# Kernel tuning notes

Measured on AMD Instinct MI355X. Metric: run time of the kernel, lower is better.

The kernel has to match this reference:

```python
import jax, jax.numpy as jnp
import numpy as np

B, S, D, H, DFF = 2, 2048, 512, 8, 2048
DH = D // H
EPS = 1e-5


def setup_inputs() -> dict:
    key = jax.random.key(0)
    ks = jax.random.split(key, 12)
    g = lambda k, shape, s=0.02: jax.random.normal(k, shape, dtype=jnp.float32) * s
    x = jax.random.normal(ks[0], (B, S, D), dtype=jnp.float32)
    # additive causal mask: 0 on/below diag, -inf above
    neg = jnp.finfo(jnp.float32).min
    attn_mask = jnp.where(jnp.tril(jnp.ones((S, S), dtype=bool)), 0.0, neg).astype(jnp.float32)
    return {
        "x": x,
        "attn_mask": attn_mask,
        "Wq": g(ks[1], (D, D)), "bq": jnp.zeros((D,), jnp.float32),
        "Wk": g(ks[2], (D, D)), "bk": jnp.zeros((D,), jnp.float32),
        "Wv": g(ks[3], (D, D)), "bv": jnp.zeros((D,), jnp.float32),
        "Wo": g(ks[4], (D, D)), "bo": jnp.zeros((D,), jnp.float32),
        "head_alphas": jnp.ones((H,), jnp.float32),
        "ln1_g": jnp.ones((D,), jnp.float32), "ln1_b": jnp.zeros((D,), jnp.float32),
        "W1": g(ks[5], (DFF, D)), "b1": jnp.zeros((DFF,), jnp.float32),
        "W2": g(ks[6], (D, DFF)), "b2": jnp.zeros((D,), jnp.float32),
        "ln2_g": jnp.ones((D,), jnp.float32), "ln2_b": jnp.zeros((D,), jnp.float32),
    }


def _layer_norm(h, g, b):
    mu = jnp.mean(h, axis=-1, keepdims=True)
    var = jnp.mean((h - mu) ** 2, axis=-1, keepdims=True)
    return (h - mu) * jax.lax.rsqrt(var + EPS) * g + b


def reference(x, attn_mask, Wq, bq, Wk, bk, Wv, bv, Wo, bo, head_alphas,
              ln1_g, ln1_b, W1, b1, W2, b2, ln2_g, ln2_b):
    scale = jnp.sqrt(jnp.asarray(DH, dtype=x.dtype))
    # projections (torch Linear: x @ W.T + b)
    q = (x @ Wq.T + bq).reshape(B, S, H, DH).transpose(0, 2, 1, 3)  # bhsd
    k = (x @ Wk.T + bk).reshape(B, S, H, DH).transpose(0, 2, 1, 3)
    v = (x @ Wv.T + bv).reshape(B, S, H, DH).transpose(0, 2, 1, 3)
    attn = jnp.einsum('bhqd,bhkd->bhqk', q, k) / scale
    attn = attn + attn_mask  # broadcast [S,S] over batch/heads
    attn = jax.nn.softmax(attn, axis=-1)
    ctx = jnp.einsum('bhqk,bhkd->bhqd', attn, v)
    ctx = ctx * head_alphas[None, :, None, None]
    ctx = ctx.transpose(0, 2, 1, 3).reshape(B, S, D)
    attn_out = ctx @ Wo.T + bo
    # residual + LN
    h = _layer_norm(x + attn_out, ln1_g, ln1_b)
    # FFN (linear -> ReLU -> linear), residual + LN
    ff = jax.nn.relu(h @ W1.T + b1) @ W2.T + b2
    out = _layer_norm(h + ff, ln2_g, ln2_b)
    return out
```

## Files before the change

kernel.cpp:

```cpp
#include <hip/hip_runtime.h>
#include <hip/hip_bf16.h>
#include <math.h>

#define BB 2
#define SS 2048
#define DD 512
#define HH 8
#define DH 64
#define DFF 2048
#define MM (BB*SS)
#define EPS 1e-5f

typedef __attribute__((ext_vector_type(8))) short bf16x8;
typedef __attribute__((ext_vector_type(4))) float f32x4;

#define GL2LDS(g, l)                                                        \
    __builtin_amdgcn_global_load_lds(                                       \
        (const __attribute__((address_space(1))) void*)(unsigned long long)(g), \
        (__attribute__((address_space(3))) void*)(unsigned int)(unsigned long long)(l), \
        16, 0, 0)

struct Cvt7 {
    const float* s[7];
    unsigned short* d[7];
    unsigned off[8];
};

__global__ __launch_bounds__(256) void cvt_k(Cvt7 a)
{
    unsigned i = blockIdx.x * 256 + threadIdx.x;
    int seg = 0;
    #pragma unroll
    for (int t = 1; t < 7; ++t) seg += (i >= a.off[t]);
    unsigned li = i - a.off[seg];
    float4 v = ((const float4*)a.s[seg])[li];
    union { __hip_bfloat16 h[4]; uint2 u; } t;
    t.h[0] = __float2bfloat16(v.x);
    t.h[1] = __float2bfloat16(v.y);
    t.h[2] = __float2bfloat16(v.z);
    t.h[3] = __float2bfloat16(v.w);
    ((uint2*)a.d[seg])[li] = t.u;
}

__global__ __launch_bounds__(256) void gemm64_k(
    const __hip_bfloat16* __restrict__ A, const __hip_bfloat16* __restrict__ Bw,
    const float* __restrict__ bias, const float* __restrict__ resid,
    void* __restrict__ Cout, int N_, int K_, int mode, float oscale)
{
    __shared__ __hip_bfloat16 As[64*64];
    __shared__ __hip_bfloat16 Bs[64*64];
    const int tid   = threadIdx.x;
    const int w     = tid >> 6;
    const int lane  = tid & 63;
    const int quad  = lane >> 4;
    const int col16 = lane & 15;
    const int m0 = blockIdx.y * 64;
    const int n0 = blockIdx.x * 64;
    const int wm = (w >> 1) * 32;
    const int wn = (w & 1) * 32;
    const int srow = lane >> 3;
    const int scol = (lane & 7) * 8;

    f32x4 acc[2][2] = {};

    for (int k0 = 0; k0 < K_; k0 += 64) {
        __syncthreads();
        #pragma unroll
        for (int t = 0; t < 4; ++t) {
            const int c = w * 4 + t;
            if (c < 8)
                GL2LDS(A  + (size_t)(m0 + c*8 + srow) * K_ + k0 + scol,
                       (char*)As + c * 1024);
            else
                GL2LDS(Bw + (size_t)(n0 + (c-8)*8 + srow) * K_ + k0 + scol,
                       (char*)Bs + (c-8) * 1024);
        }
        __syncthreads();

        #pragma unroll
        for (int kk = 0; kk < 64; kk += 32) {
            bf16x8 af[2], bf[2];
            #pragma unroll
            for (int i = 0; i < 2; ++i)
                af[i] = *(const bf16x8*)(As + (wm + i*16 + col16) * 64 + kk + quad*8);
            #pragma unroll
            for (int j = 0; j < 2; ++j)
                bf[j] = *(const bf16x8*)(Bs + (wn + j*16 + col16) * 64 + kk + quad*8);
            #pragma unroll
            for (int i = 0; i < 2; ++i)
                #pragma unroll
                for (int j = 0; j < 2; ++j)
                    acc[i][j] = __builtin_amdgcn_mfma_f32_16x16x32_bf16(
                        af[i], bf[j], acc[i][j], 0, 0, 0);
        }
    }

    #pragma unroll
    for (int i = 0; i < 2; ++i) {
        #pragma unroll
        for (int r = 0; r < 4; ++r) {
            const int m = m0 + wm + i*16 + quad*4 + r;
            #pragma unroll
            for (int j = 0; j < 2; ++j) {
                const int n = n0 + wn + j*16 + col16;
                float vv = acc[i][j][r] + bias[n];
                if (mode == 0) {
                    size_t idx = (size_t)m * N_ + n;
                    float* Cf = (float*)Cout;
                    if (resid) vv += resid[idx];
                    Cf[idx] = vv;
                } else {
                    ((__hip_bfloat16*)Cout)[(size_t)m * N_ + n] =
                        __float2bfloat16(fmaxf(vv, 0.f) * oscale);
                }
            }
        }
    }
}

__global__ __launch_bounds__(256) void gemm64sk_k(
    const __hip_bfloat16* __restrict__ A, const __hip_bfloat16* __restrict__ Bw,
    float* __restrict__ part, int N_, int Ktot, int Kseg)
{
    __shared__ __hip_bfloat16 As[64*64];
    __shared__ __hip_bfloat16 Bs[64*64];
    const int tid   = threadIdx.x;
    const int w     = tid >> 6;
    const int lane  = tid & 63;
    const int quad  = lane >> 4;
    const int col16 = lane & 15;
    const int m0 = blockIdx.y * 64;
    const int n0 = blockIdx.x * 64;
    const int wm = (w >> 1) * 32;
    const int wn = (w & 1) * 32;
    const int srow = lane >> 3;
    const int scol = (lane & 7) * 8;
    const int kbeg = blockIdx.z * Kseg;

    f32x4 acc[2][2] = {};

    for (int k0 = kbeg; k0 < kbeg + Kseg; k0 += 64) {
        __syncthreads();
        #pragma unroll
        for (int t = 0; t < 4; ++t) {
            const int c = w * 4 + t;
            if (c < 8)
                GL2LDS(A  + (size_t)(m0 + c*8 + srow) * Ktot + k0 + scol,
                       (char*)As + c * 1024);
            else
                GL2LDS(Bw + (size_t)(n0 + (c-8)*8 + srow) * Ktot + k0 + scol,
                       (char*)Bs + (c-8) * 1024);
        }
        __syncthreads();

        #pragma unroll
        for (int kk = 0; kk < 64; kk += 32) {
            bf16x8 af[2], bf[2];
            #pragma unroll
            for (int i = 0; i < 2; ++i)
                af[i] = *(const bf16x8*)(As + (wm + i*16 + col16) * 64 + kk + quad*8);
            #pragma unroll
            for (int j = 0; j < 2; ++j)
                bf[j] = *(const bf16x8*)(Bs + (wn + j*16 + col16) * 64 + kk + quad*8);
            #pragma unroll
            for (int i = 0; i < 2; ++i)
                #pragma unroll
                for (int j = 0; j < 2; ++j)
                    acc[i][j] = __builtin_amdgcn_mfma_f32_16x16x32_bf16(
                        af[i], bf[j], acc[i][j], 0, 0, 0);
        }
    }

    float* dst = part + (size_t)blockIdx.z * MM * N_;
    #pragma unroll
    for (int i = 0; i < 2; ++i)
        #pragma unroll
        for (int r = 0; r < 4; ++r) {
            const int m = m0 + wm + i*16 + quad*4 + r;
            #pragma unroll
            for (int j = 0; j < 2; ++j) {
                const int n = n0 + wn + j*16 + col16;
                dst[(size_t)m * N_ + n] = acc[i][j][r];
            }
        }
}

__global__ __launch_bounds__(256) void qkv64_k(
    const __hip_bfloat16* __restrict__ A, const __hip_bfloat16* __restrict__ Wqkv,
    const float* __restrict__ bq, const float* __restrict__ bk,
    const float* __restrict__ bv,
    __hip_bfloat16* __restrict__ qb, __hip_bfloat16* __restrict__ kb,
    __hip_bfloat16* __restrict__ vtb)
{
    __shared__ __hip_bfloat16 As[64*64];
    __shared__ __hip_bfloat16 Bs[64*64];
    const int tid   = threadIdx.x;
    const int w     = tid >> 6;
    const int lane  = tid & 63;
    const int quad  = lane >> 4;
    const int col16 = lane & 15;
    const int m0 = blockIdx.y * 64;
    const int n0 = blockIdx.x * 64;
    const int wm = (w >> 1) * 32;
    const int wn = (w & 1) * 32;
    const int srow = lane >> 3;
    const int scol = (lane & 7) * 8;

    f32x4 acc[2][2] = {};

    for (int k0 = 0; k0 < DD; k0 += 64) {
        __syncthreads();
        #pragma unroll
        for (int t = 0; t < 4; ++t) {
            const int c = w * 4 + t;
            if (c < 8)
                GL2LDS(A    + (size_t)(m0 + c*8 + srow) * DD + k0 + scol,
                       (char*)As + c * 1024);
            else
                GL2LDS(Wqkv + (size_t)(n0 + (c-8)*8 + srow) * DD + k0 + scol,
                       (char*)Bs + (c-8) * 1024);
        }
        __syncthreads();

        #pragma unroll
        for (int kk = 0; kk < 64; kk += 32) {
            bf16x8 af[2], bf[2];
            #pragma unroll
            for (int i = 0; i < 2; ++i)
                af[i] = *(const bf16x8*)(As + (wm + i*16 + col16) * 64 + kk + quad*8);
            #pragma unroll
            for (int j = 0; j < 2; ++j)
                bf[j] = *(const bf16x8*)(Bs + (wn + j*16 + col16) * 64 + kk + quad*8);
            #pragma unroll
            for (int i = 0; i < 2; ++i)
                #pragma unroll
                for (int j = 0; j < 2; ++j)
                    acc[i][j] = __builtin_amdgcn_mfma_f32_16x16x32_bf16(
                        af[i], bf[j], acc[i][j], 0, 0, 0);
        }
    }

    const int z = n0 >> 9;
    const float* bias = (z == 0) ? bq : (z == 1) ? bk : bv;
    __hip_bfloat16* dst = (z == 0) ? qb : (z == 1) ? kb : vtb;
    const float sc = (z == 0) ? 0.125f : 1.0f;
    #pragma unroll
    for (int i = 0; i < 2; ++i)
        #pragma unroll
        for (int r = 0; r < 4; ++r) {
            const int m = m0 + wm + i*16 + quad*4 + r;
            const int b = m >> 11, s = m & (SS - 1);
            #pragma unroll
            for (int j = 0; j < 2; ++j) {
                const int n  = n0 + wn + j*16 + col16;
                const int nn = n & 511;
                const int hh = nn >> 6, d = nn & (DH - 1);
                float vv = (acc[i][j][r] + bias[nn]) * sc;
                if (z < 2)
                    dst[(((size_t)(b*HH + hh))*SS + s)*DH + d] = __float2bfloat16(vv);
                else
                    dst[(((size_t)(b*HH + hh))*DH + d)*SS + s] = __float2bfloat16(vv);
            }
        }
}

__global__ __launch_bounds__(512) void attn_mfma_k(
    const __hip_bfloat16* __restrict__ Q,
    const __hip_bfloat16* __restrict__ K,
    const __hip_bfloat16* __restrict__ VT,
    const float* __restrict__ halpha,
    __hip_bfloat16* __restrict__ ctx)
{
    const int w    = threadIdx.x >> 6;
    const int lane = threadIdx.x & 63;
    const int quad = lane >> 4;
    const int col  = lane & 15;
    const int bh   = blockIdx.x;
    const int b    = bh >> 3, h = bh & 7;
    const int qt   = gridDim.y - 1 - blockIdx.y;
    const int q0   = qt * 64;
    const int nchunk = qt + 1;

    const __hip_bfloat16* Qbh = Q  + (size_t)bh * SS * DH;
    const __hip_bfloat16* Kbh = K  + (size_t)bh * SS * DH;
    const __hip_bfloat16* Vbh = VT + (size_t)bh * DH * SS;

    __shared__ float smem[16896];
    __hip_bfloat16* bb     = (__hip_bfloat16*)smem;
    __hip_bfloat16* p_base = bb + (size_t)w * 4096;
    float* lbuf = smem + 16384;

    bf16x8 qf[4][2];
    #pragma unroll
    for (int mi = 0; mi < 4; ++mi) {
        const __hip_bfloat16* qp = Qbh + (size_t)(q0 + mi*16 + col) * DH + quad * 8;
        qf[mi][0] = *(const bf16x8*)(qp);
        qf[mi][1] = *(const bf16x8*)(qp + 32);
    }

    f32x4 acc_o[4][4] = {};
    float lp[4][4] = {};

    for (int c = w; c < nchunk; c += 8) {
        const int k0 = c * 64;
        const bool diag = (c == qt);

        #pragma unroll
        for (int ks = 0; ks < 4; ++ks) {
            const __hip_bfloat16* kp = Kbh + (size_t)(k0 + ks*16 + col) * DH + quad * 8;
            bf16x8 kb0 = *(const bf16x8*)(kp);
            bf16x8 kb1 = *(const bf16x8*)(kp + 32);
            const int keyl = ks*16 + col;
            const int kh = keyl >> 5;
            const int lr = ((keyl >> 3) & 3) * 16;
            const int j  = keyl & 7;
            const int kg = k0 + keyl;
            #pragma unroll
            for (int mi = 0; mi < 4; ++mi) {
                f32x4 s = {};
                s = __builtin_amdgcn_mfma_f32_16x16x32_bf16(qf[mi][0], kb0, s, 0, 0, 0);
                s = __builtin_amdgcn_mfma_f32_16x16x32_bf16(qf[mi][1], kb1, s, 0, 0, 0);
                #pragma unroll
                for (int r = 0; r < 4; ++r) {
                    float p;
                    if (diag) {
                        int qg = q0 + mi*16 + quad*4 + r;
                        p = (kg > qg) ? 0.f : __expf(s[r]);
                    } else {
                        p = __expf(s[r]);
                    }
                    lp[mi][r] += p;
                    p_base[mi*1024 + kh*512 + (lr + quad*4 + r)*8 + j] =
                        __float2bfloat16(p);
                }
            }
        }

        bf16x8 pa[4][2];
        #pragma unroll
        for (int mi = 0; mi < 4; ++mi) {
            pa[mi][0] = *(const bf16x8*)(p_base + mi*1024 + lane*8);
            pa[mi][1] = *(const bf16x8*)(p_base + mi*1024 + 512 + lane*8);
        }
        #pragma unroll
        for (int d = 0; d < 4; ++d) {
            const __hip_bfloat16* vp = Vbh + (size_t)(d*16 + col) * SS + k0 + quad * 8;
            bf16x8 vb0 = *(const bf16x8*)(vp);
            bf16x8 vb1 = *(const bf16x8*)(vp + 32);
            #pragma unroll
            for (int mi = 0; mi < 4; ++mi) {
                acc_o[mi][d] = __builtin_amdgcn_mfma_f32_16x16x32_bf16(pa[mi][0], vb0, acc_o[mi][d], 0, 0, 0);
                acc_o[mi][d] = __builtin_amdgcn_mfma_f32_16x16x32_bf16(pa[mi][1], vb1, acc_o[mi][d], 0, 0, 0);
            }
        }
    }

    #pragma unroll
    for (int mi = 0; mi < 4; ++mi)
        #pragma unroll
        for (int r = 0; r < 4; ++r) {
            float s_ = lp[mi][r];
            #pragma unroll
            for (int o = 1; o < 16; o <<= 1) s_ += __shfl_xor(s_, o);
            lp[mi][r] = s_;
        }

    __syncthreads();
    __hip_bfloat16* obuf = bb + (size_t)w * 4096;
    #pragma unroll
    for (int mi = 0; mi < 4; ++mi)
        #pragma unroll
        for (int d = 0; d < 4; ++d)
            #pragma unroll
            for (int r = 0; r < 4; ++r)
                obuf[(mi*16 + quad*4 + r)*64 + d*16 + col] =
                    __float2bfloat16(acc_o[mi][d][r]);
    if (col == 0) {
        #pragma unroll
        for (int mi = 0; mi < 4; ++mi)
            #pragma unroll
            for (int r = 0; r < 4; ++r)
                lbuf[w*64 + mi*16 + quad*4 + r] = lp[mi][r];
    }
    __syncthreads();

    const float ha = halpha[h];
    #pragma unroll
    for (int rr = 0; rr < 8; ++rr) {
        const int row = w*8 + rr;
        float L = 0.f, val = 0.f;
        #pragma unroll
        for (int p = 0; p < 8; ++p) {
            L   += lbuf[p*64 + row];
            val += __bfloat162float(bb[p*4096 + row*64 + lane]);
        }
        ctx[((size_t)(b*SS + q0 + row))*DD + h*64 + lane] =
            __float2bfloat16(val * ha / L);
    }
}

__global__ __launch_bounds__(256) void ln_red_k(
    const float* __restrict__ pa, const float* __restrict__ pb,
    const float* __restrict__ bias, const float* __restrict__ resid,
    const float* __restrict__ g, const float* __restrict__ bta,
    float* __restrict__ out, __hip_bfloat16* __restrict__ outb)
{
    const int row = blockIdx.x;
    const size_t base = (size_t)row * DD;
    const int t = threadIdx.x;
    float v0 = pa[base + t]       + pb[base + t]       + bias[t]       + resid[base + t];
    float v1 = pa[base + t + 256] + pb[base + t + 256] + bias[t + 256] + resid[base + t + 256];
    __shared__ float red[256];
    red[t] = v0 + v1;
    __syncthreads();
    for (int o = 128; o > 0; o >>= 1) { if (t < o) red[t] += red[t + o]; __syncthreads(); }
    float mu = red[0] * (1.f / DD);
    __syncthreads();
    float d0 = v0 - mu, d1 = v1 - mu;
    red[t] = d0*d0 + d1*d1;
    __syncthreads();
    for (int o = 128; o > 0; o >>= 1) { if (t < o) red[t] += red[t + o]; __syncthreads(); }
    float rstd = rsqrtf(red[0] * (1.f / DD) + EPS);
    float o0 = d0 * rstd * g[t]       + bta[t];
    float o1 = d1 * rstd * g[t + 256] + bta[t + 256];
    out[base + t]       = o0;
    out[base + t + 256] = o1;
    if (outb) {
        outb[base + t]       = __float2bfloat16(o0);
        outb[base + t + 256] = __float2bfloat16(o1);
    }
}

extern "C" void kernel_launch(void* const* d_in, const int* in_sizes, int n_in,
                              void* d_out, int out_size, void* d_ws, size_t ws_size,
                              hipStream_t stream)
{
    const float* x    = (const float*)d_in[0];
    const float* Wq   = (const float*)d_in[2];
    const float* bq   = (const float*)d_in[3];
    const float* Wk   = (const float*)d_in[4];
    const float* bk   = (const float*)d_in[5];
    const float* Wv   = (const float*)d_in[6];
    const float* bv   = (const float*)d_in[7];
    const float* Wo   = (const float*)d_in[8];
    const float* bo   = (const float*)d_in[9];
    const float* hal  = (const float*)d_in[10];
    const float* ln1g = (const float*)d_in[11];
    const float* ln1b = (const float*)d_in[12];
    const float* W1   = (const float*)d_in[13];
    const float* b1   = (const float*)d_in[14];
    const float* W2   = (const float*)d_in[15];
    const float* b2   = (const float*)d_in[16];
    const float* ln2g = (const float*)d_in[17];
    const float* ln2b = (const float*)d_in[18];
    float* out = (float*)d_out;

    char* ws = (char*)d_ws;
    const size_t MB = 1ull << 20;
    __hip_bfloat16* Wqkv = (__hip_bfloat16*)(ws);
    __hip_bfloat16* Wob  = (__hip_bfloat16*)(ws + MB + MB/2);
    __hip_bfloat16* W1b  = (__hip_bfloat16*)(ws + 2*MB);
    __hip_bfloat16* W2b  = (__hip_bfloat16*)(ws + 4*MB);
    __hip_bfloat16* xb   = (__hip_bfloat16*)(ws + 6*MB);
    __hip_bfloat16* qb   = (__hip_bfloat16*)(ws + 10*MB);
    __hip_bfloat16* kb   = (__hip_bfloat16*)(ws + 14*MB);
    __hip_bfloat16* vtb  = (__hip_bfloat16*)(ws + 18*MB);
    __hip_bfloat16* ctxb = (__hip_bfloat16*)(ws + 22*MB);
    float* part = (float*)(ws + 26*MB);
    float* h    = (float*)(ws + 42*MB);
    __hip_bfloat16* hb   = (__hip_bfloat16*)(ws + 22*MB);
    __hip_bfloat16* ff1b = (__hip_bfloat16*)(ws + 6*MB);

    dim3 blk(256);
    const size_t PSEG = (size_t)MM * DD;

    Cvt7 ca;
    ca.s[0] = x;  ca.d[0] = (unsigned short*)xb;
    ca.s[1] = Wq; ca.d[1] = (unsigned short*)Wqkv;
    ca.s[2] = Wk; ca.d[2] = (unsigned short*)(Wqkv + 512*512);
    ca.s[3] = Wv; ca.d[3] = (unsigned short*)(Wqkv + 2*512*512);
    ca.s[4] = Wo; ca.d[4] = (unsigned short*)Wob;
    ca.s[5] = W1; ca.d[5] = (unsigned short*)W1b;
    ca.s[6] = W2; ca.d[6] = (unsigned short*)W2b;
    unsigned offs[8] = {0, 524288, 589824, 655360, 720896, 786432, 1048576, 1310720};
    for (int i = 0; i < 8; ++i) ca.off[i] = offs[i];
    cvt_k<<<dim3(5120), blk, 0, stream>>>(ca);

    qkv64_k<<<dim3((3*DD)/64, MM/64), blk, 0, stream>>>(
        xb, Wqkv, bq, bk, bv, qb, kb, vtb);

    attn_mfma_k<<<dim3(BB*HH, SS/64), dim3(512), 0, stream>>>(
        qb, kb, vtb, hal, ctxb);

    gemm64sk_k<<<dim3(DD/64, MM/64, 2), blk, 0, stream>>>(
        ctxb, Wob, part, DD, DD, 256);
    ln_red_k<<<dim3(MM), blk, 0, stream>>>(
        part, part + PSEG, bo, x, ln1g, ln1b, h, hb);

    gemm64_k<<<dim3(DFF/64, MM/64), blk, 0, stream>>>(
        hb, W1b, b1, nullptr, ff1b, DFF, DD, 3, 1.0f);

    gemm64sk_k<<<dim3(DD/64, MM/64, 2), blk, 0, stream>>>(
        ff1b, W2b, part, DD, DFF, 1024);
    ln_red_k<<<dim3(MM), blk, 0, stream>>>(
        part, part + PSEG, b2, h, ln2g, ln2b, out, nullptr);
}
```

Measured before the change: 237.4 us.

## Replace 64x64 GEMMs with weight-resident LDS kernel streaming activations from global

Three GEMM kernels become one kernel. Each block loads a 64x512 weight slice once into LDS, using rotated chunks to avoid bank conflicts, then computes a 256-row tile with 4x4 MFMA accumulators per wave. Activation fragments are read directly from global memory instead of LDS. The goal is to remove the repeated per-k-step LDS staging and barrier sync of the old tiles and to reuse weights across more rows. In exchange, the out-projection drops its split-K, the W2 GEMM moves to a 4-way split, the LN reduction now takes a variable partial count, and direct global A loads may be poorly coalesced.

```diff
diff --git a/kernel.cpp b/kernel.cpp
--- a/kernel.cpp
+++ b/kernel.cpp
@@ -10,6 +10,7 @@
 #define DFF 2048
 #define MM (BB*SS)
 #define EPS 1e-5f
+#define PSEG ((size_t)MM * DD)
 
 typedef __attribute__((ext_vector_type(8))) short bf16x8;
 typedef __attribute__((ext_vector_type(4))) float f32x4;
@@ -42,226 +43,106 @@
     ((uint2*)a.d[seg])[li] = t.u;
 }
 
-__global__ __launch_bounds__(256) void gemm64_k(
-    const __hip_bfloat16* __restrict__ A, const __hip_bfloat16* __restrict__ Bw,
-    const float* __restrict__ bias, const float* __restrict__ resid,
-    void* __restrict__ Cout, int N_, int K_, int mode, float oscale)
-{
-    __shared__ __hip_bfloat16 As[64*64];
-    __shared__ __hip_bfloat16 Bs[64*64];
+__global__ __launch_bounds__(256) void gemm_wres_k(
+    const __hip_bfloat16* __restrict__ A, const __hip_bfloat16* __restrict__ W,
+    const float* __restrict__ bias, void* __restrict__ dst,
+    __hip_bfloat16* __restrict__ qdst, __hip_bfloat16* __restrict__ kdst,
+    __hip_bfloat16* __restrict__ vdst,
+    const float* __restrict__ bq, const float* __restrict__ bk,
+    const float* __restrict__ bv,
+    int N_, int Ktot, int mode)
+{
+    __shared__ __hip_bfloat16 Ws[64 * 512];
     const int tid   = threadIdx.x;
     const int w     = tid >> 6;
     const int lane  = tid & 63;
     const int quad  = lane >> 4;
     const int col16 = lane & 15;
-    const int m0 = blockIdx.y * 64;
     const int n0 = blockIdx.x * 64;
-    const int wm = (w >> 1) * 32;
-    const int wn = (w & 1) * 32;
-    const int srow = lane >> 3;
-    const int scol = (lane & 7) * 8;
-
-    f32x4 acc[2][2] = {};
-
-    for (int k0 = 0; k0 < K_; k0 += 64) {
-        __syncthreads();
-        #pragma unroll
-        for (int t = 0; t < 4; ++t) {
-            const int c = w * 4 + t;
-            if (c < 8)
-                GL2LDS(A  + (size_t)(m0 + c*8 + srow) * K_ + k0 + scol,
-                       (char*)As + c * 1024);
-            else
-                GL2LDS(Bw + (size_t)(n0 + (c-8)*8 + srow) * K_ + k0 + scol,
-                       (char*)Bs + (c-8) * 1024);
-        }
-        __syncthreads();
-
-        #pragma unroll
-        for (int kk = 0; kk < 64; kk += 32) {
-            bf16x8 af[2], bf[2];
-            #pragma unroll
-            for (int i = 0; i < 2; ++i)
-                af[i] = *(const bf16x8*)(As + (wm + i*16 + col16) * 64 + kk + quad*8);
-            #pragma unroll
-            for (int j = 0; j < 2; ++j)
-                bf[j] = *(const bf16x8*)(Bs + (wn + j*16 + col16) * 64 + kk + quad*8);
-            #pragma unroll
-            for (int i = 0; i < 2; ++i)
+    const int m0 = blockIdx.y * 256;
+    const int kbase = blockIdx.z * 512;
+
+    #pragma unroll
+    for (int i = 0; i < 16; ++i) {
+        const int row = w * 16 + i;
+        const int rot = row & 7;
+        const int src = ((lane + rot) & 63) * 8;
+        GL2LDS(W + (size_t)(n0 + row) * Ktot + kbase + src, Ws + row * 512);
+    }
+    __syncthreads();
+
+    const int mw = m0 + w * 64;
+    f32x4 acc[4][4] = {};
+    #pragma unroll 2
+    for (int ks = 0; ks < 16; ++ks) {
+        bf16x8 af[4], wf[4];
+        #pragma unroll
+        for (int mi = 0; mi < 4; ++mi)
+            af[mi] = *(const bf16x8*)(A + (size_t)(mw + mi*16 + col16) * Ktot
+                                        + kbase + ks*32 + quad*8);
+        #pragma unroll
+        for (int nj = 0; nj < 4; ++nj) {
+            const int row = nj*16 + col16;
+            const int chunk = (ks*4 + quad - (col16 & 7)) & 63;
+            wf[nj] = *(const bf16x8*)(Ws + row * 512 + chunk * 8);
+        }
+        #pragma unroll
+        for (int mi = 0; mi < 4; ++mi)
+            #pragma unroll
+            for (int nj = 0; nj < 4; ++nj)
+                acc[mi][nj] = __builtin_amdgcn_mfma_f32_16x16x32_bf16(
+                    af[mi], wf[nj], acc[mi][nj], 0, 0, 0);
+    }
+
+    if (mode == 0) {
+        float* part = (float*)dst + (size_t)blockIdx.z * MM * N_;
+        #pragma unroll
+        for (int mi = 0; mi < 4; ++mi)
+            #pragma unroll
+            for (int r = 0; r < 4; ++r) {
+                const int m = mw + mi*16 + quad*4 + r;
                 #pragma unroll
-                for (int j = 0; j < 2; ++j)
-                    acc[i][j] = __builtin_amdgcn_mfma_f32_16x16x32_bf16(
-                        af[i], bf[j], acc[i][j], 0, 0, 0);
-        }
-    }
-
-    #pragma unroll
-    for (int i = 0; i < 2; ++i) {
-        #pragma unroll
-        for (int r = 0; r < 4; ++r) {
-            const int m = m0 + wm + i*16 + quad*4 + r;
-            #pragma unroll
-            for (int j = 0; j < 2; ++j) {
-                const int n = n0 + wn + j*16 + col16;
-                float vv = acc[i][j][r] + bias[n];
-                if (mode == 0) {
-                    size_t idx = (size_t)m * N_ + n;
-                    float* Cf = (float*)Cout;
-                    if (resid) vv += resid[idx];
-                    Cf[idx] = vv;
-                } else {
-                    ((__hip_bfloat16*)Cout)[(size_t)m * N_ + n] =
-                        __float2bfloat16(fmaxf(vv, 0.f) * oscale);
+                for (int nj = 0; nj < 4; ++nj)
+                    part[(size_t)m * N_ + n0 + nj*16 + col16] = acc[mi][nj][r];
+            }
+    } else if (mode == 3) {
+        __hip_bfloat16* o = (__hip_bfloat16*)dst;
+        #pragma unroll
+        for (int mi = 0; mi < 4; ++mi)
+            #pragma unroll
+            for (int r = 0; r < 4; ++r) {
+                const int m = mw + mi*16 + quad*4 + r;
+                #pragma unroll
+                for (int nj = 0; nj < 4; ++nj) {
+                    const int n = n0 + nj*16 + col16;
+                    o[(size_t)m * N_ + n] =
+                        __float2bfloat16(fmaxf(acc[mi][nj][r] + bias[n], 0.f));
                 }
             }
-        }
-    }
-}
-
-__global__ __launch_bounds__(256) void gemm64sk_k(
-    const __hip_bfloat16* __restrict__ A, const __hip_bfloat16* __restrict__ Bw,
-    float* __restrict__ part, int N_, int Ktot, int Kseg)
-{
-    __shared__ __hip_bfloat16 As[64*64];
-    __shared__ __hip_bfloat16 Bs[64*64];
-    const int tid   = threadIdx.x;
-    const int w     = tid >> 6;
-    const int lane  = tid & 63;
-    const int quad  = lane >> 4;
-    const int col16 = lane & 15;
-    const int m0 = blockIdx.y * 64;
-    const int n0 = blockIdx.x * 64;
-    const int wm = (w >> 1) * 32;
-    const int wn = (w & 1) * 32;
-    const int srow = lane >> 3;
-    const int scol = (lane & 7) * 8;
-    const int kbeg = blockIdx.z * Kseg;
-
-    f32x4 acc[2][2] = {};
-
-    for (int k0 = kbeg; k0 < kbeg + Kseg; k0 += 64) {
-        __syncthreads();
-        #pragma unroll
-        for (int t = 0; t < 4; ++t) {
-            const int c = w * 4 + t;
-            if (c < 8)
-                GL2LDS(A  + (size_t)(m0 + c*8 + srow) * Ktot + k0 + scol,
-                       (char*)As + c * 1024);
-            else
-                GL2LDS(Bw + (size_t)(n0 + (c-8)*8 + srow) * Ktot + k0 + scol,
-                       (char*)Bs + (c-8) * 1024);
-        }
-        __syncthreads();
-
-        #pragma unroll
-        for (int kk = 0; kk < 64; kk += 32) {
-            bf16x8 af[2], bf[2];
-            #pragma unroll
-            for (int i = 0; i < 2; ++i)
-                af[i] = *(const bf16x8*)(As + (wm + i*16 + col16) * 64 + kk + quad*8);
-            #pragma unroll
-            for (int j = 0; j < 2; ++j)
-                bf[j] = *(const bf16x8*)(Bs + (wn + j*16 + col16) * 64 + kk + quad*8);
-            #pragma unroll
-            for (int i = 0; i < 2; ++i)
+    } else {
+        const int z = n0 >> 9;
+        const float* bi = (z == 0) ? bq : (z == 1) ? bk : bv;
+        __hip_bfloat16* o = (z == 0) ? qdst : (z == 1) ? kdst : vdst;
+        const float sc = (z == 0) ? 0.125f : 1.0f;
+        #pragma unroll
+        for (int mi = 0; mi < 4; ++mi)
+            #pragma unroll
+            for (int r = 0; r < 4; ++r) {
+                const int m = mw + mi*16 + quad*4 + r;
+                const int b = m >> 11, s = m & (SS - 1);
                 #pragma unroll
-                for (int j = 0; j < 2; ++j)
-                    acc[i][j] = __builtin_amdgcn_mfma_f32_16x16x32_bf16(
-                        af[i], bf[j], acc[i][j], 0, 0, 0);
-        }
-    }
-
-    float* dst = part + (size_t)blockIdx.z * MM * N_;
-    #pragma unroll
-    for (int i = 0; i < 2; ++i)
-        #pragma unroll
-        for (int r = 0; r < 4; ++r) {
-            const int m = m0 + wm + i*16 + quad*4 + r;
-            #pragma unroll
-            for (int j = 0; j < 2; ++j) {
-                const int n = n0 + wn + j*16 + col16;
-                dst[(size_t)m * N_ + n] = acc[i][j][r];
-            }
-        }
-}
-
-__global__ __launch_bounds__(256) void qkv64_k(
-    const __hip_bfloat16* __restrict__ A, const __hip_bfloat16* __restrict__ Wqkv,
-    const float* __restrict__ bq, const float* __restrict__ bk,
-    const float* __restrict__ bv,
-    __hip_bfloat16* __restrict__ qb, __hip_bfloat16* __restrict__ kb,
-    __hip_bfloat16* __restrict__ vtb)
-{
-    __shared__ __hip_bfloat16 As[64*64];
-    __shared__ __hip_bfloat16 Bs[64*64];
-    const int tid   = threadIdx.x;
-    const int w     = tid >> 6;
-    const int lane  = tid & 63;
-    const int quad  = lane >> 4;
-    const int col16 = lane & 15;
-    const int m0 = blockIdx.y * 64;
-    const int n0 = blockIdx.x * 64;
-    const int wm = (w >> 1) * 32;
-    const int wn = (w & 1) * 32;
-    const int srow = lane >> 3;
-    const int scol = (lane & 7) * 8;
-
-    f32x4 acc[2][2] = {};
-
-    for (int k0 = 0; k0 < DD; k0 += 64) {
-        __syncthreads();
-        #pragma unroll
-        for (int t = 0; t < 4; ++t) {
-            const int c = w * 4 + t;
-            if (c < 8)
-                GL2LDS(A    + (size_t)(m0 + c*8 + srow) * DD + k0 + scol,
-                       (char*)As + c * 1024);
-            else
-                GL2LDS(Wqkv + (size_t)(n0 + (c-8)*8 + srow) * DD + k0 + scol,
-                       (char*)Bs + (c-8) * 1024);
-        }
-        __syncthreads();
-
-        #pragma unroll
-        for (int kk = 0; kk < 64; kk += 32) {
-            bf16x8 af[2], bf[2];
-            #pragma unroll
-            for (int i = 0; i < 2; ++i)
-                af[i] = *(const bf16x8*)(As + (wm + i*16 + col16) * 64 + kk + quad*8);
-            #pragma unroll
-            for (int j = 0; j < 2; ++j)
-                bf[j] = *(const bf16x8*)(Bs + (wn + j*16 + col16) * 64 + kk + quad*8);
-            #pragma unroll
-            for (int i = 0; i < 2; ++i)
-                #pragma unroll
-                for (int j = 0; j < 2; ++j)
-                    acc[i][j] = __builtin_amdgcn_mfma_f32_16x16x32_bf16(
-                        af[i], bf[j], acc[i][j], 0, 0, 0);
-        }
-    }
-
-    const int z = n0 >> 9;
-    const float* bias = (z == 0) ? bq : (z == 1) ? bk : bv;
-    __hip_bfloat16* dst = (z == 0) ? qb : (z == 1) ? kb : vtb;
-    const float sc = (z == 0) ? 0.125f : 1.0f;
-    #pragma unroll
-    for (int i = 0; i < 2; ++i)
-        #pragma unroll
-        for (int r = 0; r < 4; ++r) {
-            const int m = m0 + wm + i*16 + quad*4 + r;
-            const int b = m >> 11, s = m & (SS - 1);
-            #pragma unroll
-            for (int j = 0; j < 2; ++j) {
-                const int n  = n0 + wn + j*16 + col16;
-                const int nn = n & 511;
-                const int hh = nn >> 6, d = nn & (DH - 1);
-                float vv = (acc[i][j][r] + bias[nn]) * sc;
-                if (z < 2)
-                    dst[(((size_t)(b*HH + hh))*SS + s)*DH + d] = __float2bfloat16(vv);
-                else
-                    dst[(((size_t)(b*HH + hh))*DH + d)*SS + s] = __float2bfloat16(vv);
-            }
-        }
+                for (int nj = 0; nj < 4; ++nj) {
+                    const int n  = n0 + nj*16 + col16;
+                    const int nn = n & 511;
+                    const int hh = nn >> 6, d = nn & (DH - 1);
+                    float vv = (acc[mi][nj][r] + bi[nn]) * sc;
+                    if (z < 2)
+                        o[(((size_t)(b*HH + hh))*SS + s)*DH + d] = __float2bfloat16(vv);
+                    else
+                        o[(((size_t)(b*HH + hh))*DH + d)*SS + s] = __float2bfloat16(vv);
+                }
+            }
+    }
 }
 
 __global__ __launch_bounds__(512) void attn_mfma_k(
@@ -400,7 +281,7 @@
 }
 
 __global__ __launch_bounds__(256) void ln_red_k(
-    const float* __restrict__ pa, const float* __restrict__ pb,
+    const float* __restrict__ parts, int np,
     const float* __restrict__ bias, const float* __restrict__ resid,
     const float* __restrict__ g, const float* __restrict__ bta,
     float* __restrict__ out, __hip_bfloat16* __restrict__ outb)
@@ -408,8 +289,12 @@
     const int row = blockIdx.x;
     const size_t base = (size_t)row * DD;
     const int t = threadIdx.x;
-    float v0 = pa[base + t]       + pb[base + t]       + bias[t]       + resid[base + t];
-    float v1 = pa[base + t + 256] + pb[base + t + 256] + bias[t + 256] + resid[base + t + 256];
+    float v0 = bias[t]       + resid[base + t];
+    float v1 = bias[t + 256] + resid[base + t + 256];
+    for (int p = 0; p < np; ++p) {
+        v0 += parts[p * PSEG + base + t];
+        v1 += parts[p * PSEG + base + t + 256];
+    }
     __shared__ float red[256];
     red[t] = v0 + v1;
     __syncthreads();
@@ -467,12 +352,11 @@
     __hip_bfloat16* vtb  = (__hip_bfloat16*)(ws + 18*MB);
     __hip_bfloat16* ctxb = (__hip_bfloat16*)(ws + 22*MB);
     float* part = (float*)(ws + 26*MB);
-    float* h    = (float*)(ws + 42*MB);
+    float* h    = (float*)(ws + 58*MB);
     __hip_bfloat16* hb   = (__hip_bfloat16*)(ws + 22*MB);
     __hip_bfloat16* ff1b = (__hip_bfloat16*)(ws + 6*MB);
 
     dim3 blk(256);
-    const size_t PSEG = (size_t)MM * DD;
 
     Cvt7 ca;
     ca.s[0] = x;  ca.d[0] = (unsigned short*)xb;
@@ -486,22 +370,25 @@
     for (int i = 0; i < 8; ++i) ca.off[i] = offs[i];
     cvt_k<<<dim3(5120), blk, 0, stream>>>(ca);
 
-    qkv64_k<<<dim3((3*DD)/64, MM/64), blk, 0, stream>>>(
-        xb, Wqkv, bq, bk, bv, qb, kb, vtb);
+    gemm_wres_k<<<dim3(24, 16), blk, 0, stream>>>(
+        xb, Wqkv, nullptr, nullptr, qb, kb, vtb, bq, bk, bv, DD, DD, 1);
 
     attn_mfma_k<<<dim3(BB*HH, SS/64), dim3(512), 0, stream>>>(
         qb, kb, vtb, hal, ctxb);
 
-    gemm64sk_k<<<dim3(DD/64, MM/64, 2), blk, 0, stream>>>(
-        ctxb, Wob, part, DD, DD, 256);
+    gemm_wres_k<<<dim3(8, 16), blk, 0, stream>>>(
+        ctxb, Wob, nullptr, part, nullptr, nullptr, nullptr,
+        nullptr, nullptr, nullptr, DD, DD, 0);
     ln_red_k<<<dim3(MM), blk, 0, stream>>>(
-        part, part + PSEG, bo, x, ln1g, ln1b, h, hb);
-
-    gemm64_k<<<dim3(DFF/64, MM/64), blk, 0, stream>>>(
-        hb, W1b, b1, nullptr, ff1b, DFF, DD, 3, 1.0f);
-
-    gemm64sk_k<<<dim3(DD/64, MM/64, 2), blk, 0, stream>>>(
-        ff1b, W2b, part, DD, DFF, 1024);
+        part, 1, bo, x, ln1g, ln1b, h, hb);
+
+    gemm_wres_k<<<dim3(32, 16), blk, 0, stream>>>(
+        hb, W1b, b1, ff1b, nullptr, nullptr, nullptr,
+        nullptr, nullptr, nullptr, DFF, DD, 3);
+
+    gemm_wres_k<<<dim3(8, 16, 4), blk, 0, stream>>>(
+        ff1b, W2b, nullptr, part, nullptr, nullptr, nullptr,
+        nullptr, nullptr, nullptr, DD, DFF, 0);
     ln_red_k<<<dim3(MM), blk, 0, stream>>>(
-        part, part + PSEG, b2, h, ln2g, ln2b, out, nullptr);
-}
+        part, 4, b2, h, ln2g, ln2b, out, nullptr);
+}
```

Measured after the change: 258.7 us. 9.0% more time.
